# Optimization experiments

Hardware: AMD Instinct MI355X
Metric: run time of the kernel (lower is better)

Reference implementation:

```python
import jax, jax.numpy as jnp
import numpy as np

B, S, NX, H = 8, 1024, 1024, 16
D = NX // H  # head_features = 64
SCALE = True


def setup_inputs() -> dict:
    key = jax.random.key(0)
    k1, k2, k3 = jax.random.split(key, 3)
    x = jax.random.normal(k1, (B, S, NX), dtype=jnp.float32)
    w_attn = jax.random.normal(k2, (NX, 3 * NX), dtype=jnp.float32) * 0.02
    b_attn = jnp.zeros((3 * NX,), dtype=jnp.float32)
    w_proj = jax.random.normal(k3, (NX, NX), dtype=jnp.float32) * 0.02
    b_proj = jnp.zeros((NX,), dtype=jnp.float32)
    return {"x": x, "w_attn": w_attn, "b_attn": b_attn, "w_proj": w_proj, "b_proj": b_proj}


def _split_heads(t):
    # (B, S, NX) -> (B, H, S, D)
    return t.reshape(B, S, H, D).transpose(0, 2, 1, 3)


def reference(x, w_attn, b_attn, w_proj, b_proj):
    # fused QKV projection (Conv1D): addmm over flattened tokens
    qkv = x @ w_attn + b_attn                      # (B, S, 3*NX)
    q, k, v = jnp.split(qkv, 3, axis=-1)
    q = _split_heads(q)                            # (B, H, S, D)
    k = _split_heads(k)
    v = _split_heads(v)

    w = jnp.einsum("bhqd,bhkd->bhqk", q, k)        # full S x S scores
    if SCALE:
        w = w / jnp.sqrt(jnp.asarray(D, w.dtype))
    # causal mask applied exactly as in the source: multiply + big-negative subtract
    b = jnp.tril(jnp.ones((S, S), dtype=w.dtype))[None, None]
    w = w * b - 1e10 * (1.0 - b)
    w = jax.nn.softmax(w, axis=-1)                 # attn_pdrop = 0 (eval)
    a = jnp.einsum("bhqk,bhkd->bhqd", w, v)        # (B, H, S, D)

    # merge heads: (B, H, S, D) -> (B, S, NX)
    a = a.transpose(0, 2, 1, 3).reshape(B, S, NX)
    a = a @ w_proj + b_proj                        # c_proj; resid_pdrop = 0 (eval)
    return a
```

## Files before the change

kernel.cpp:

```cpp
#include <hip/hip_runtime.h>
#include <hip/hip_bf16.h>

#define BB 8
#define SS 1024
#define NXX 1024
#define HH 16
#define DD 64
#define MM (BB * SS)

typedef __attribute__((ext_vector_type(8))) short short8;
typedef __attribute__((ext_vector_type(4))) short short4v;
typedef __attribute__((ext_vector_type(4))) float float4v;

static __device__ inline short bf16bits(float v) {
    __hip_bfloat16 t = __float2bfloat16(v);
    return *reinterpret_cast<short*>(&t);
}

__global__ __launch_bounds__(256) void prep_kernel(
    const float* __restrict__ x, __hip_bfloat16* __restrict__ xb,
    const float* __restrict__ w_attn, __hip_bfloat16* __restrict__ wT_attn,
    const float* __restrict__ w_proj, __hip_bfloat16* __restrict__ wT_proj)
{
    __shared__ __hip_bfloat16 tile[32][33];
    const int blk = blockIdx.x;
    const int tid = threadIdx.x;

    if (blk < 8192) {
        int i = blk * 1024 + tid * 4;
        float4 v = *(const float4*)(x + i);
        xb[i + 0] = __float2bfloat16(v.x);
        xb[i + 1] = __float2bfloat16(v.y);
        xb[i + 2] = __float2bfloat16(v.z);
        xb[i + 3] = __float2bfloat16(v.w);
        return;
    }
    const float* W;
    __hip_bfloat16* Wt;
    int K, N, idx;
    if (blk < 8192 + 3072) { idx = blk - 8192;  W = w_attn; Wt = wT_attn; K = NXX; N = 3 * NXX; }
    else                   { idx = blk - 11264; W = w_proj; Wt = wT_proj; K = NXX; N = NXX; }
    const int k0 = (idx % (K / 32)) * 32;
    const int n0 = (idx / (K / 32)) * 32;
    const int tx = tid % 32;
    const int ty = tid / 32;
#pragma unroll
    for (int p = 0; p < 4; ++p) {
        int k = ty + p * 8;
        tile[k][tx] = __float2bfloat16(W[(size_t)(k0 + k) * N + n0 + tx]);
    }
    __syncthreads();
#pragma unroll
    for (int p = 0; p < 4; ++p) {
        int nn = ty + p * 8;
        Wt[(size_t)(n0 + nn) * K + k0 + tx] = tile[tx][nn];
    }
}

#define STAGE_A(DST, kk)                                                       \
    {                                                                          \
        _Pragma("unroll") for (int j_ = 0; j_ < LA; ++j_) {                    \
            const __hip_bfloat16* s_ = aSrc + (size_t)(j_ * 128) * K + (kk);   \
            char* d_ = (char*)(DST) + j_ * 8192 + (wave << 10);                \
            __builtin_amdgcn_global_load_lds(                                  \
                (const __attribute__((address_space(1))) void*)s_,             \
                (__attribute__((address_space(3))) void*)d_, 16, 0, 0);        \
        }                                                                      \
    }

#define STAGE_B(DST, kk)                                                       \
    {                                                                          \
        _Pragma("unroll") for (int j_ = 0; j_ < LB; ++j_) {                    \
            const __hip_bfloat16* s_ = bSrc + (size_t)(j_ * 128) * K + (kk);   \
            char* d_ = (char*)(DST) + j_ * 8192 + (wave << 10);                \
            __builtin_amdgcn_global_load_lds(                                  \
                (const __attribute__((address_space(1))) void*)s_,             \
                (__attribute__((address_space(3))) void*)d_, 16, 0, 0);        \
        }                                                                      \
    }

#define WAIT_LGKM0_FENCED()                                                    \
    asm volatile("s_waitcnt lgkmcnt(0)" ::: "memory");                         \
    __builtin_amdgcn_sched_barrier(0);

#define WAIT_VMCNT_LT()                                                        \
    if constexpr (LT == 3) { asm volatile("s_waitcnt vmcnt(3)" ::: "memory"); }\
    else                   { asm volatile("s_waitcnt vmcnt(2)" ::: "memory"); }

template <int MODE, int BM, int BN>
__global__ __launch_bounds__(512, 2) void gemm256(
    const __hip_bfloat16* __restrict__ A,
    const __hip_bfloat16* __restrict__ Bt,
    const float* __restrict__ bias,
    void* __restrict__ Cv,
    __hip_bfloat16* __restrict__ vT,
    int M, int K, int N)
{
    constexpr int NWM = BM / 64;
    constexpr int NWN = 8 / NWM;
    constexpr int WCOLS = BN / NWN;
    constexpr int NF = WCOLS / 16;
    constexpr int ASZ = BM * 64;
    constexpr int BSZ = BN * 64;
    constexpr int LA = BM / 128;
    constexpr int LB = BN / 128;
    constexpr int LT = LA + LB;

    __shared__ __attribute__((aligned(16))) char smem[3 * ASZ + 2 * BSZ];

    const int tid  = threadIdx.x;
    const int wave = tid >> 6;
    const int lane = tid & 63;
    const int wm = (wave / NWN) * 64;
    const int wn = (wave % NWN) * WCOLS;

    const int nwg = (int)gridDim.x;
    const int cpx = nwg >> 3;
    const int bid = (int)blockIdx.x;
    const int swz = (bid & 7) * cpx + (bid >> 3);
    const int ntN = N / BN;
    const int width = ntN << 3;
    const int group = swz / width;
    const int w = swz % width;
    const int m0 = (group * 8 + (w & 7)) * BM;
    const int n0 = (w >> 3) * BN;

    const int NT = K >> 5;

    const int row_s  = tid >> 2;
    const int srccol = (((tid & 3) ^ ((tid >> 3) & 3)) << 3);
    const __hip_bfloat16* aSrc = A  + (size_t)(m0 + row_s) * K + srccol;
    const __hip_bfloat16* bSrc = Bt + (size_t)(n0 + row_s) * K + srccol;

    const int l15 = lane & 15, q4 = lane >> 4;
    const int sslot = (q4 ^ ((l15 >> 1) & 3)) << 4;
    const int offA = (wm + l15) * 64 + sslot;
    const int offB = (wn + l15) * 64 + sslot;

    float4v acc[4][NF];
#pragma unroll
    for (int i = 0; i < 4; ++i)
#pragma unroll
        for (int j = 0; j < NF; ++j) acc[i][j] = (float4v){0.f, 0.f, 0.f, 0.f};

    char* const Abuf0 = (char*)smem;
    char* const Bbuf0 = (char*)smem + 3 * ASZ;

    STAGE_A(Abuf0,       0);
    STAGE_B(Bbuf0,       0);
    STAGE_A(Abuf0 + ASZ, 32);
    STAGE_B(Bbuf0 + BSZ, 32);
    WAIT_VMCNT_LT();
    __builtin_amdgcn_s_barrier();

    int ia = 0;
    for (int t = 0; t < NT; ++t) {
        const char* Ab = Abuf0 + ia * ASZ;
        char* Bb = Bbuf0 + (t & 1) * BSZ;
        const int ia2 = (ia == 0) ? 2 : ia - 1;

        short8 a[4], b[NF];

#pragma unroll
        for (int mf = 0; mf < 2; ++mf) a[mf] = *(const short8*)(Ab + offA + mf * 1024);
#pragma unroll
        for (int nf = 0; nf < NF; ++nf) b[nf] = *(const short8*)(Bb + offB + nf * 1024);
        if (t + 2 < NT) STAGE_A(Abuf0 + ia2 * ASZ, (t + 2) << 5);
        __builtin_amdgcn_s_barrier();
        WAIT_LGKM0_FENCED();
        __builtin_amdgcn_s_setprio(1);
#pragma unroll
        for (int mf = 0; mf < 2; ++mf)
#pragma unroll
            for (int nf = 0; nf < NF; ++nf)
                acc[mf][nf] = __builtin_amdgcn_mfma_f32_16x16x32_bf16(
                    a[mf], b[nf], acc[mf][nf], 0, 0, 0);
        __builtin_amdgcn_s_setprio(0);
        __builtin_amdgcn_s_barrier();

#pragma unroll
        for (int mf = 2; mf < 4; ++mf) a[mf] = *(const short8*)(Ab + offA + mf * 1024);
        if (t + 2 < NT) {
            STAGE_B(Bb, (t + 2) << 5);
            WAIT_VMCNT_LT();
        } else if (t + 1 < NT) {
            asm volatile("s_waitcnt vmcnt(0)" ::: "memory");
        }
        __builtin_amdgcn_s_barrier();
        WAIT_LGKM0_FENCED();
        __builtin_amdgcn_s_setprio(1);
#pragma unroll
        for (int mf = 2; mf < 4; ++mf)
#pragma unroll
            for (int nf = 0; nf < NF; ++nf)
                acc[mf][nf] = __builtin_amdgcn_mfma_f32_16x16x32_bf16(
                    a[mf], b[nf], acc[mf][nf], 0, 0, 0);
        __builtin_amdgcn_s_setprio(0);
        __builtin_amdgcn_s_barrier();

        ia = (ia == 2) ? 0 : ia + 1;
    }

    const int cr = q4 * 4;
    const int cc = l15;

    if (MODE == 1 && n0 >= 2048) {
        const int bb = m0 / SS;
#pragma unroll
        for (int mf = 0; mf < 4; ++mf) {
            int grow = m0 + wm + mf * 16 + cr;
            int ssr = grow & (SS - 1);
#pragma unroll
            for (int nf = 0; nf < NF; ++nf) {
                int gcol = n0 + wn + nf * 16 + cc;
                float bv = bias[gcol];
                int col = gcol - 2048;
                int hh = col >> 6, dd = col & 63;
                short4v pk;
#pragma unroll
                for (int r = 0; r < 4; ++r) pk[r] = bf16bits(acc[mf][nf][r] + bv);
                *(short4v*)(vT + (size_t)((bb * HH + hh) * 64 + dd) * SS + ssr) = pk;
            }
        }
    } else {
        const float qs = (MODE == 1 && n0 < 1024) ? 0.125f : 1.0f;
#pragma unroll
        for (int mf = 0; mf < 4; ++mf) {
            int grow = m0 + wm + mf * 16 + cr;
#pragma unroll
            for (int nf = 0; nf < NF; ++nf) {
                int gcol = n0 + wn + nf * 16 + cc;
                float bv = bias[gcol];
#pragma unroll
                for (int r = 0; r < 4; ++r) {
                    float v = (acc[mf][nf][r] + bv) * qs;
                    if constexpr (MODE == 1)
                        ((__hip_bfloat16*)Cv)[(size_t)(grow + r) * N + gcol] =
                            __float2bfloat16(v);
                    else
                        ((float*)Cv)[(size_t)(grow + r) * N + gcol] = v;
                }
            }
        }
    }
}

#define PSTR 72

__global__ __launch_bounds__(256) void attn_mfma_kernel(
    const __hip_bfloat16* __restrict__ qkv,
    const __hip_bfloat16* __restrict__ vT,
    __hip_bfloat16* __restrict__ aout)
{
    const int bh = blockIdx.x;
    const int b = bh / HH, h = bh % HH;
    const int q0 = ((int)gridDim.y - 1 - (int)blockIdx.y) * 128;

    __shared__ __hip_bfloat16 Ks[64 * PSTR];
    __shared__ __hip_bfloat16 Vs[64 * PSTR];
    __shared__ __hip_bfloat16 Ps[4][32 * PSTR];

    const int tid  = threadIdx.x;
    const int wave = tid >> 6;
    const int lane = tid & 63;
    const int quad = lane >> 4;
    const int l16  = lane & 15;

    short8 qf[2][2];
#pragma unroll
    for (int t = 0; t < 2; ++t) {
        const __hip_bfloat16* qp = qkv +
            (size_t)(b * SS + q0 + wave * 32 + t * 16 + l16) * 3072 + h * 64 + quad * 8;
        qf[t][0] = *(const short8*)qp;
        qf[t][1] = *(const short8*)(qp + 32);
    }

    float4v o_acc[2][4];
    float l_acc[2][4];
#pragma unroll
    for (int t = 0; t < 2; ++t)
#pragma unroll
        for (int nt = 0; nt < 4; ++nt) o_acc[t][nt] = (float4v){0.f, 0.f, 0.f, 0.f};
#pragma unroll
    for (int t = 0; t < 2; ++t)
#pragma unroll
        for (int r = 0; r < 4; ++r) l_acc[t][r] = 0.f;

    const int sk  = tid & 63;
    const int sdo = (tid >> 6) * 16;
    const int vd  = tid >> 2;
    const int vko = (tid & 3) * 16;
    const int qmin_w = q0 + wave * 32;
    const int nkt = q0 / 64 + 2;

    for (int kt = 0; kt < nkt; ++kt) {
        const int k0 = kt * 64;
        __syncthreads();
        {
            const __hip_bfloat16* kr =
                qkv + (size_t)(b * SS + k0 + sk) * 3072 + 1024 + h * 64 + sdo;
            *(short8*)&Ks[sk * PSTR + sdo]     = *(const short8*)kr;
            *(short8*)&Ks[sk * PSTR + sdo + 8] = *(const short8*)(kr + 8);
            const __hip_bfloat16* vr = vT + (size_t)(bh * 64 + vd) * SS + k0 + vko;
            *(short8*)&Vs[vd * PSTR + vko]     = *(const short8*)vr;
            *(short8*)&Vs[vd * PSTR + vko + 8] = *(const short8*)(vr + 8);
        }
        __syncthreads();
        if (k0 > qmin_w + 31) continue;

        const short* ks = (const short*)Ks;
        float4v sacc[2][4];
#pragma unroll
        for (int t = 0; t < 2; ++t)
#pragma unroll
            for (int nt = 0; nt < 4; ++nt) sacc[t][nt] = (float4v){0.f, 0.f, 0.f, 0.f};
#pragma unroll
        for (int kc = 0; kc < 2; ++kc)
#pragma unroll
            for (int nt = 0; nt < 4; ++nt) {
                short8 kb = *(const short8*)(ks + (nt * 16 + l16) * PSTR + kc * 32 + quad * 8);
                sacc[0][nt] = __builtin_amdgcn_mfma_f32_16x16x32_bf16(qf[0][kc], kb, sacc[0][nt], 0, 0, 0);
                sacc[1][nt] = __builtin_amdgcn_mfma_f32_16x16x32_bf16(qf[1][kc], kb, sacc[1][nt], 0, 0, 0);
            }

        const bool needmask = (k0 + 63 > qmin_w);
        __hip_bfloat16* pw = Ps[wave];
#pragma unroll
        for (int t = 0; t < 2; ++t)
#pragma unroll
            for (int nt = 0; nt < 4; ++nt) {
                int kk = k0 + nt * 16 + l16;
#pragma unroll
                for (int r = 0; r < 4; ++r) {
                    float s = sacc[t][nt][r];
                    if (needmask) {
                        int qq = qmin_w + t * 16 + quad * 4 + r;
                        if (kk > qq) s = -1e10f;
                    }
                    float p = __expf(s);
                    l_acc[t][r] += p;
                    pw[(t * 16 + quad * 4 + r) * PSTR + nt * 16 + l16] =
                        __float2bfloat16(p);
                }
            }

        const short* ps = (const short*)pw;
        const short* vs = (const short*)Vs;
#pragma unroll
        for (int kc = 0; kc < 2; ++kc) {
            short8 pa0 = *(const short8*)(ps + (0 * 16 + l16) * PSTR + kc * 32 + quad * 8);
            short8 pa1 = *(const short8*)(ps + (1 * 16 + l16) * PSTR + kc * 32 + quad * 8);
#pragma unroll
            for (int nt = 0; nt < 4; ++nt) {
                short8 vb = *(const short8*)(vs + (nt * 16 + l16) * PSTR + kc * 32 + quad * 8);
                o_acc[0][nt] = __builtin_amdgcn_mfma_f32_16x16x32_bf16(pa0, vb, o_acc[0][nt], 0, 0, 0);
                o_acc[1][nt] = __builtin_amdgcn_mfma_f32_16x16x32_bf16(pa1, vb, o_acc[1][nt], 0, 0, 0);
            }
        }
    }

#pragma unroll
    for (int t = 0; t < 2; ++t)
#pragma unroll
        for (int r = 0; r < 4; ++r) {
            float l = l_acc[t][r];
            l += __shfl_xor(l, 1);
            l += __shfl_xor(l, 2);
            l += __shfl_xor(l, 4);
            l += __shfl_xor(l, 8);
            float inv = 1.f / l;
            int row = q0 + wave * 32 + t * 16 + quad * 4 + r;
            __hip_bfloat16* op = aout + (size_t)(b * SS + row) * NXX + h * 64 + l16;
#pragma unroll
            for (int nt = 0; nt < 4; ++nt)
                op[nt * 16] = __float2bfloat16(o_acc[t][nt][r] * inv);
        }
}

extern "C" void kernel_launch(void* const* d_in, const int* in_sizes, int n_in,
                              void* d_out, int out_size, void* d_ws, size_t ws_size,
                              hipStream_t stream)
{
    const float* x      = (const float*)d_in[0];
    const float* w_attn = (const float*)d_in[1];
    const float* b_attn = (const float*)d_in[2];
    const float* w_proj = (const float*)d_in[3];
    const float* b_proj = (const float*)d_in[4];
    float* out = (float*)d_out;

    char* ws = (char*)d_ws;
    __hip_bfloat16* qkv     = (__hip_bfloat16*)ws;
    __hip_bfloat16* vT      = (__hip_bfloat16*)(ws + (size_t)48 * 1024 * 1024);
    __hip_bfloat16* xb      = (__hip_bfloat16*)(ws + (size_t)64 * 1024 * 1024);
    __hip_bfloat16* amid    = xb;
    __hip_bfloat16* wT_attn = (__hip_bfloat16*)(ws + (size_t)80 * 1024 * 1024);
    __hip_bfloat16* wT_proj = (__hip_bfloat16*)(ws + (size_t)86 * 1024 * 1024);

    prep_kernel<<<dim3(12288), dim3(256), 0, stream>>>(
        x, xb, w_attn, wT_attn, w_proj, wT_proj);

    gemm256<1, 256, 128><<<dim3((MM / 256) * ((3 * NXX) / 128)), dim3(512), 0, stream>>>(
        xb, wT_attn, b_attn, qkv, vT, MM, NXX, 3 * NXX);

    attn_mfma_kernel<<<dim3(BB * HH, SS / 128), dim3(256), 0, stream>>>(qkv, vT, amid);

    gemm256<0, 128, 128><<<dim3((MM / 128) * (NXX / 128)), dim3(512), 0, stream>>>(
        amid, wT_proj, b_proj, out, nullptr, MM, NXX, NXX);
}
```

Baseline: 221.7 us.

## Add 256x256 ping-pong GEMM for QKV projection and enlarge proj tile

Adds a new gemm8k kernel that computes 256x256 output tiles with 128KB of dynamic LDS, double-buffered global_load_lds staging, interleaved quarter-step MFMA phases with barriers and setprio, and an XCD-aware block swizzle. It replaces the 256x128 QKV projection GEMM when the dynamic shared-memory attribute can be set. The output projection switches from 128x128 to 256x128 tiles. The aim is more operand reuse per LDS load and better overlap of loads with MFMA; the cost is fewer workgroups, possibly lower occupancy, and more barriers per iteration.

```diff
diff --git a/kernel.cpp b/kernel.cpp
--- a/kernel.cpp
+++ b/kernel.cpp
@@ -57,6 +57,10 @@
     }
 }
 
+#define WAIT_LGKM0_FENCED()                                                    \
+    asm volatile("s_waitcnt lgkmcnt(0)" ::: "memory");                         \
+    __builtin_amdgcn_sched_barrier(0);
+
 #define STAGE_A(DST, kk)                                                       \
     {                                                                          \
         _Pragma("unroll") for (int j_ = 0; j_ < LA; ++j_) {                    \
@@ -78,10 +82,6 @@
                 (__attribute__((address_space(3))) void*)d_, 16, 0, 0);        \
         }                                                                      \
     }
-
-#define WAIT_LGKM0_FENCED()                                                    \
-    asm volatile("s_waitcnt lgkmcnt(0)" ::: "memory");                         \
-    __builtin_amdgcn_sched_barrier(0);
 
 #define WAIT_VMCNT_LT()                                                        \
     if constexpr (LT == 3) { asm volatile("s_waitcnt vmcnt(3)" ::: "memory"); }\
@@ -245,6 +245,203 @@
     }
 }
 
+#define STAGE8(SRCBASE, DST, half, kk)                                         \
+    {                                                                          \
+        _Pragma("unroll") for (int j_ = 0; j_ < 2; ++j_) {                     \
+            const __hip_bfloat16* s_ =                                         \
+                (SRCBASE) + (size_t)((half) * 128 + j_ * 64) * K + (kk);       \
+            char* d_ = (char*)(DST) + (half) * 16384 + j_ * 8192 + (wave << 10); \
+            __builtin_amdgcn_global_load_lds(                                  \
+                (const __attribute__((address_space(1))) void*)s_,             \
+                (__attribute__((address_space(3))) void*)d_, 16, 0, 0);        \
+        }                                                                      \
+    }
+
+template <int MODE>
+__global__ __launch_bounds__(512, 2) void gemm8k(
+    const __hip_bfloat16* __restrict__ A,
+    const __hip_bfloat16* __restrict__ Bt,
+    const float* __restrict__ bias,
+    void* __restrict__ Cv,
+    __hip_bfloat16* __restrict__ vT,
+    int M, int K, int N)
+{
+    extern __shared__ char smem[];
+
+    const int tid  = threadIdx.x;
+    const int wave = tid >> 6;
+    const int lane = tid & 63;
+    const int wr = wave >> 2;
+    const int wc = wave & 3;
+
+    const int nwg = (int)gridDim.x;
+    const int cpx = nwg >> 3;
+    const int bid = (int)blockIdx.x;
+    const int swz = (bid & 7) * cpx + (bid >> 3);
+    const int ntN = N >> 8;
+    const int width = ntN << 3;
+    const int group = swz / width;
+    const int w = swz % width;
+    const int m0 = ((group << 3) + (w & 7)) << 8;
+    const int n0 = (w >> 3) << 8;
+
+    const int NT = K >> 6;
+
+    const int row_s  = tid >> 3;
+    const int slot_s = tid & 7;
+    const int srccol = ((slot_s ^ (row_s & 7)) << 3);
+    const __hip_bfloat16* aSrc = A  + (size_t)(m0 + row_s) * K + srccol;
+    const __hip_bfloat16* bSrc = Bt + (size_t)(n0 + row_s) * K + srccol;
+
+    const int l15 = lane & 15, q4 = lane >> 4, xr = lane & 7;
+    const int sl0 = (q4 ^ xr) << 4;
+    const int sl1 = ((4 + q4) ^ xr) << 4;
+    const int offA0 = ((wr << 7) + l15) * 128 + sl0;
+    const int offA1 = ((wr << 7) + l15) * 128 + sl1;
+    const int offB0 = ((wc << 6) + l15) * 128 + sl0;
+    const int offB1 = ((wc << 6) + l15) * 128 + sl1;
+
+    float4v acc[8][4];
+#pragma unroll
+    for (int i = 0; i < 8; ++i)
+#pragma unroll
+        for (int j = 0; j < 4; ++j) acc[i][j] = (float4v){0.f, 0.f, 0.f, 0.f};
+
+    STAGE8(aSrc, smem, 0, 0);
+    STAGE8(aSrc, smem, 1, 0);
+    STAGE8(bSrc, smem + 32768, 0, 0);
+    STAGE8(bSrc, smem + 32768, 1, 0);
+    if (NT > 1) {
+        STAGE8(bSrc, smem + 65536 + 32768, 0, 64);
+        STAGE8(bSrc, smem + 65536 + 32768, 1, 64);
+        asm volatile("s_waitcnt vmcnt(4)" ::: "memory");
+    } else {
+        asm volatile("s_waitcnt vmcnt(0)" ::: "memory");
+    }
+    __builtin_amdgcn_s_barrier();
+
+    for (int t = 0; t < NT; ++t) {
+        const char* Ab = smem + ((t & 1) << 16);
+        const char* Bb = Ab + 32768;
+        char* AbN = (char*)smem + (((t + 1) & 1) << 16);
+        char* BbC = (char*)Ab + 32768;
+
+        short8 a0[4], a1[4], b0[4], b1[4];
+
+#pragma unroll
+        for (int mf = 0; mf < 4; ++mf) a0[mf] = *(const short8*)(Ab + offA0 + mf * 2048);
+#pragma unroll
+        for (int nf = 0; nf < 4; ++nf) b0[nf] = *(const short8*)(Bb + offB0 + nf * 2048);
+        if (t + 1 < NT) STAGE8(aSrc, AbN, 0, (t + 1) << 6);
+        __builtin_amdgcn_s_barrier();
+        WAIT_LGKM0_FENCED();
+        __builtin_amdgcn_s_setprio(1);
+#pragma unroll
+        for (int mf = 0; mf < 4; ++mf)
+#pragma unroll
+            for (int nf = 0; nf < 4; ++nf)
+                acc[mf][nf] = __builtin_amdgcn_mfma_f32_16x16x32_bf16(
+                    a0[mf], b0[nf], acc[mf][nf], 0, 0, 0);
+        __builtin_amdgcn_s_setprio(0);
+        __builtin_amdgcn_s_barrier();
+
+#pragma unroll
+        for (int mf = 0; mf < 4; ++mf) a1[mf] = *(const short8*)(Ab + offA1 + mf * 2048);
+#pragma unroll
+        for (int nf = 0; nf < 4; ++nf) b1[nf] = *(const short8*)(Bb + offB1 + nf * 2048);
+        if (t + 1 < NT) STAGE8(aSrc, AbN, 1, (t + 1) << 6);
+        __builtin_amdgcn_s_barrier();
+        WAIT_LGKM0_FENCED();
+        __builtin_amdgcn_s_setprio(1);
+#pragma unroll
+        for (int mf = 0; mf < 4; ++mf)
+#pragma unroll
+            for (int nf = 0; nf < 4; ++nf)
+                acc[mf][nf] = __builtin_amdgcn_mfma_f32_16x16x32_bf16(
+                    a1[mf], b1[nf], acc[mf][nf], 0, 0, 0);
+        __builtin_amdgcn_s_setprio(0);
+        __builtin_amdgcn_s_barrier();
+
+#pragma unroll
+        for (int mf = 0; mf < 4; ++mf) a0[mf] = *(const short8*)(Ab + offA0 + (mf + 4) * 2048);
+        if (t + 2 < NT) STAGE8(bSrc, BbC, 0, (t + 2) << 6);
+        __builtin_amdgcn_s_barrier();
+        WAIT_LGKM0_FENCED();
+        __builtin_amdgcn_s_setprio(1);
+#pragma unroll
+        for (int mf = 0; mf < 4; ++mf)
+#pragma unroll
+            for (int nf = 0; nf < 4; ++nf)
+                acc[mf + 4][nf] = __builtin_amdgcn_mfma_f32_16x16x32_bf16(
+                    a0[mf], b0[nf], acc[mf + 4][nf], 0, 0, 0);
+        __builtin_amdgcn_s_setprio(0);
+        __builtin_amdgcn_s_barrier();
+
+#pragma unroll
+        for (int mf = 0; mf < 4; ++mf) a1[mf] = *(const short8*)(Ab + offA1 + (mf + 4) * 2048);
+        if (t + 2 < NT) {
+            STAGE8(bSrc, BbC, 1, (t + 2) << 6);
+            asm volatile("s_waitcnt vmcnt(4)" ::: "memory");
+        } else if (t + 1 < NT) {
+            asm volatile("s_waitcnt vmcnt(0)" ::: "memory");
+        }
+        __builtin_amdgcn_s_barrier();
+        WAIT_LGKM0_FENCED();
+        __builtin_amdgcn_s_setprio(1);
+#pragma unroll
+        for (int mf = 0; mf < 4; ++mf)
+#pragma unroll
+            for (int nf = 0; nf < 4; ++nf)
+                acc[mf + 4][nf] = __builtin_amdgcn_mfma_f32_16x16x32_bf16(
+                    a1[mf], b1[nf], acc[mf + 4][nf], 0, 0, 0);
+        __builtin_amdgcn_s_setprio(0);
+        __builtin_amdgcn_s_barrier();
+    }
+
+    const int cr = q4 * 4;
+    const int cc = l15;
+
+    if (MODE == 1 && n0 >= 2048) {
+        const int bb = m0 / SS;
+#pragma unroll
+        for (int mf = 0; mf < 8; ++mf) {
+            int grow = m0 + (wr << 7) + mf * 16 + cr;
+            int ssr = grow & (SS - 1);
+#pragma unroll
+            for (int nf = 0; nf < 4; ++nf) {
+                int gcol = n0 + (wc << 6) + nf * 16 + cc;
+                float bv = bias[gcol];
+                int col = gcol - 2048;
+                int hh = col >> 6, dd = col & 63;
+                short4v pk;
+#pragma unroll
+                for (int r = 0; r < 4; ++r) pk[r] = bf16bits(acc[mf][nf][r] + bv);
+                *(short4v*)(vT + (size_t)((bb * HH + hh) * 64 + dd) * SS + ssr) = pk;
+            }
+        }
+    } else {
+        const float qs = (MODE == 1 && n0 < 1024) ? 0.125f : 1.0f;
+#pragma unroll
+        for (int mf = 0; mf < 8; ++mf) {
+            int grow = m0 + (wr << 7) + mf * 16 + cr;
+#pragma unroll
+            for (int nf = 0; nf < 4; ++nf) {
+                int gcol = n0 + (wc << 6) + nf * 16 + cc;
+                float bv = bias[gcol];
+#pragma unroll
+                for (int r = 0; r < 4; ++r) {
+                    float v = (acc[mf][nf][r] + bv) * qs;
+                    if constexpr (MODE == 1)
+                        ((__hip_bfloat16*)Cv)[(size_t)(grow + r) * N + gcol] =
+                            __float2bfloat16(v);
+                    else
+                        ((float*)Cv)[(size_t)(grow + r) * N + gcol] = v;
+                }
+            }
+        }
+    }
+}
+
 #define PSTR 72
 
 __global__ __launch_bounds__(256) void attn_mfma_kernel(
@@ -396,14 +593,28 @@
     __hip_bfloat16* wT_attn = (__hip_bfloat16*)(ws + (size_t)80 * 1024 * 1024);
     __hip_bfloat16* wT_proj = (__hip_bfloat16*)(ws + (size_t)86 * 1024 * 1024);
 
+    static int dyn_state = 0;
+    if (dyn_state == 0) {
+        hipError_t e = hipFuncSetAttribute(
+            reinterpret_cast<const void*>(&gemm8k<1>),
+            hipFuncAttributeMaxDynamicSharedMemorySize, 131072);
+        dyn_state = (e == hipSuccess) ? 1 : -1;
+        (void)hipGetLastError();
+    }
+
     prep_kernel<<<dim3(12288), dim3(256), 0, stream>>>(
         x, xb, w_attn, wT_attn, w_proj, wT_proj);
 
-    gemm256<1, 256, 128><<<dim3((MM / 256) * ((3 * NXX) / 128)), dim3(512), 0, stream>>>(
-        xb, wT_attn, b_attn, qkv, vT, MM, NXX, 3 * NXX);
+    if (dyn_state == 1) {
+        gemm8k<1><<<dim3((MM / 256) * ((3 * NXX) / 256)), dim3(512), 131072, stream>>>(
+            xb, wT_attn, b_attn, qkv, vT, MM, NXX, 3 * NXX);
+    } else {
+        gemm256<1, 256, 128><<<dim3((MM / 256) * ((3 * NXX) / 128)), dim3(512), 0, stream>>>(
+            xb, wT_attn, b_attn, qkv, vT, MM, NXX, 3 * NXX);
+    }
 
     attn_mfma_kernel<<<dim3(BB * HH, SS / 128), dim3(256), 0, stream>>>(qkv, vT, amid);
 
-    gemm256<0, 128, 128><<<dim3((MM / 128) * (NXX / 128)), dim3(512), 0, stream>>>(
+    gemm256<0, 256, 128><<<dim3((MM / 256) * (NXX / 128)), dim3(512), 0, stream>>>(
         amid, wT_proj, b_proj, out, nullptr, MM, NXX, NXX);
 }
```

Measured after the change: 229.6 us. 1.04x slower.

## Add triple-buffered dynamic-LDS GEMM with single barrier pair per K-step

Applied to the files above, without the earlier changes.

Introduces a new GEMM kernel that uses three LDS stages, allocated as dynamic shared memory, prefetching two K-tiles ahead through global_load_lds. Each K-tile is loaded into registers before the next prefetch is issued, which aims to hide global memory latency better than the previous pipeline. The output projection also switches from 128x128 to 256x128 tiles, halving its grid. The larger LDS footprint may limit blocks per CU, and the runtime falls back to the old kernel if the attribute call fails.

```diff
diff --git a/kernel.cpp b/kernel.cpp
--- a/kernel.cpp
+++ b/kernel.cpp
@@ -57,6 +57,10 @@
     }
 }
 
+#define WAIT_LGKM0_FENCED()                                                    \
+    asm volatile("s_waitcnt lgkmcnt(0)" ::: "memory");                         \
+    __builtin_amdgcn_sched_barrier(0);
+
 #define STAGE_A(DST, kk)                                                       \
     {                                                                          \
         _Pragma("unroll") for (int j_ = 0; j_ < LA; ++j_) {                    \
@@ -79,9 +83,148 @@
         }                                                                      \
     }
 
-#define WAIT_LGKM0_FENCED()                                                    \
-    asm volatile("s_waitcnt lgkmcnt(0)" ::: "memory");                         \
-    __builtin_amdgcn_sched_barrier(0);
+template <int MODE, int BM, int BN>
+__global__ __launch_bounds__(512, 2) void gemm3b(
+    const __hip_bfloat16* __restrict__ A,
+    const __hip_bfloat16* __restrict__ Bt,
+    const float* __restrict__ bias,
+    void* __restrict__ Cv,
+    __hip_bfloat16* __restrict__ vT,
+    int M, int K, int N)
+{
+    constexpr int NWM = BM / 64;
+    constexpr int NWN = 8 / NWM;
+    constexpr int WCOLS = BN / NWN;
+    constexpr int NF = WCOLS / 16;
+    constexpr int ASZ = BM * 64;
+    constexpr int BSZ = BN * 64;
+    constexpr int LA = BM / 128;
+    constexpr int LB = BN / 128;
+
+    extern __shared__ __attribute__((aligned(16))) char smem[];
+
+    const int tid  = threadIdx.x;
+    const int wave = tid >> 6;
+    const int lane = tid & 63;
+    const int wm = (wave / NWN) * 64;
+    const int wn = (wave % NWN) * WCOLS;
+
+    const int nwg = (int)gridDim.x;
+    const int cpx = nwg >> 3;
+    const int bid = (int)blockIdx.x;
+    const int swz = (bid & 7) * cpx + (bid >> 3);
+    const int ntN = N / BN;
+    const int width = ntN << 3;
+    const int group = swz / width;
+    const int w = swz % width;
+    const int m0 = (group * 8 + (w & 7)) * BM;
+    const int n0 = (w >> 3) * BN;
+
+    const int NT = K >> 5;
+
+    const int row_s  = tid >> 2;
+    const int srccol = (((tid & 3) ^ ((tid >> 3) & 3)) << 3);
+    const __hip_bfloat16* aSrc = A  + (size_t)(m0 + row_s) * K + srccol;
+    const __hip_bfloat16* bSrc = Bt + (size_t)(n0 + row_s) * K + srccol;
+
+    const int l15 = lane & 15, q4 = lane >> 4;
+    const int sslot = (q4 ^ ((l15 >> 1) & 3)) << 4;
+    const int offA = (wm + l15) * 64 + sslot;
+    const int offB = (wn + l15) * 64 + sslot;
+
+    float4v acc[4][NF];
+#pragma unroll
+    for (int i = 0; i < 4; ++i)
+#pragma unroll
+        for (int j = 0; j < NF; ++j) acc[i][j] = (float4v){0.f, 0.f, 0.f, 0.f};
+
+    char* const Abuf0 = (char*)smem;
+    char* const Bbuf0 = (char*)smem + 3 * ASZ;
+
+    STAGE_A(Abuf0,       0);
+    STAGE_B(Bbuf0,       0);
+    STAGE_A(Abuf0 + ASZ, 32);
+    STAGE_B(Bbuf0 + BSZ, 32);
+    asm volatile("s_waitcnt vmcnt(3)" ::: "memory");
+    __builtin_amdgcn_s_barrier();
+
+    int ia = 0;
+    for (int t = 0; t < NT; ++t) {
+        const char* Ab = Abuf0 + ia * ASZ;
+        const char* Bb = Bbuf0 + ia * BSZ;
+        const int ia2 = (ia >= 1) ? ia - 1 : 2;
+
+        short8 a[4], b[NF];
+#pragma unroll
+        for (int mf = 0; mf < 4; ++mf) a[mf] = *(const short8*)(Ab + offA + mf * 1024);
+#pragma unroll
+        for (int nf = 0; nf < NF; ++nf) b[nf] = *(const short8*)(Bb + offB + nf * 1024);
+
+        if (t + 2 < NT) {
+            STAGE_A(Abuf0 + ia2 * ASZ, (t + 2) << 5);
+            STAGE_B(Bbuf0 + ia2 * BSZ, (t + 2) << 5);
+            asm volatile("s_waitcnt vmcnt(3)" ::: "memory");
+        } else if (t + 1 < NT) {
+            asm volatile("s_waitcnt vmcnt(0)" ::: "memory");
+        }
+        __builtin_amdgcn_s_barrier();
+        WAIT_LGKM0_FENCED();
+        __builtin_amdgcn_s_setprio(1);
+#pragma unroll
+        for (int mf = 0; mf < 4; ++mf)
+#pragma unroll
+            for (int nf = 0; nf < NF; ++nf)
+                acc[mf][nf] = __builtin_amdgcn_mfma_f32_16x16x32_bf16(
+                    a[mf], b[nf], acc[mf][nf], 0, 0, 0);
+        __builtin_amdgcn_s_setprio(0);
+        __builtin_amdgcn_s_barrier();
+
+        ia = (ia == 2) ? 0 : ia + 1;
+    }
+
+    const int cr = q4 * 4;
+    const int cc = l15;
+
+    if (MODE == 1 && n0 >= 2048) {
+        const int bb = m0 / SS;
+#pragma unroll
+        for (int mf = 0; mf < 4; ++mf) {
+            int grow = m0 + wm + mf * 16 + cr;
+            int ssr = grow & (SS - 1);
+#pragma unroll
+            for (int nf = 0; nf < NF; ++nf) {
+                int gcol = n0 + wn + nf * 16 + cc;
+                float bv = bias[gcol];
+                int col = gcol - 2048;
+                int hh = col >> 6, dd = col & 63;
+                short4v pk;
+#pragma unroll
+                for (int r = 0; r < 4; ++r) pk[r] = bf16bits(acc[mf][nf][r] + bv);
+                *(short4v*)(vT + (size_t)((bb * HH + hh) * 64 + dd) * SS + ssr) = pk;
+            }
+        }
+    } else {
+        const float qs = (MODE == 1 && n0 < 1024) ? 0.125f : 1.0f;
+#pragma unroll
+        for (int mf = 0; mf < 4; ++mf) {
+            int grow = m0 + wm + mf * 16 + cr;
+#pragma unroll
+            for (int nf = 0; nf < NF; ++nf) {
+                int gcol = n0 + wn + nf * 16 + cc;
+                float bv = bias[gcol];
+#pragma unroll
+                for (int r = 0; r < 4; ++r) {
+                    float v = (acc[mf][nf][r] + bv) * qs;
+                    if constexpr (MODE == 1)
+                        ((__hip_bfloat16*)Cv)[(size_t)(grow + r) * N + gcol] =
+                            __float2bfloat16(v);
+                    else
+                        ((float*)Cv)[(size_t)(grow + r) * N + gcol] = v;
+                }
+            }
+        }
+    }
+}
 
 #define WAIT_VMCNT_LT()                                                        \
     if constexpr (LT == 3) { asm volatile("s_waitcnt vmcnt(3)" ::: "memory"); }\
@@ -396,14 +539,39 @@
     __hip_bfloat16* wT_attn = (__hip_bfloat16*)(ws + (size_t)80 * 1024 * 1024);
     __hip_bfloat16* wT_proj = (__hip_bfloat16*)(ws + (size_t)86 * 1024 * 1024);
 
+    constexpr int DYN_LDS = 3 * (256 * 64) + 3 * (128 * 64);
+    static int dyn_state = 0;
+    if (dyn_state == 0) {
+        hipError_t e1 = hipFuncSetAttribute(
+            reinterpret_cast<const void*>(&gemm3b<1, 256, 128>),
+            hipFuncAttributeMaxDynamicSharedMemorySize, DYN_LDS);
+        hipError_t e2 = hipFuncSetAttribute(
+            reinterpret_cast<const void*>(&gemm3b<0, 256, 128>),
+            hipFuncAttributeMaxDynamicSharedMemorySize, DYN_LDS);
+        dyn_state = (e1 == hipSuccess && e2 == hipSuccess) ? 1 : -1;
+        (void)hipGetLastError();
+    }
+
     prep_kernel<<<dim3(12288), dim3(256), 0, stream>>>(
         x, xb, w_attn, wT_attn, w_proj, wT_proj);
 
-    gemm256<1, 256, 128><<<dim3((MM / 256) * ((3 * NXX) / 128)), dim3(512), 0, stream>>>(
-        xb, wT_attn, b_attn, qkv, vT, MM, NXX, 3 * NXX);
+    if (dyn_state == 1) {
+        gemm3b<1, 256, 128><<<dim3((MM / 256) * ((3 * NXX) / 128)), dim3(512),
+                              DYN_LDS, stream>>>(
+            xb, wT_attn, b_attn, qkv, vT, MM, NXX, 3 * NXX);
+    } else {
+        gemm256<1, 256, 128><<<dim3((MM / 256) * ((3 * NXX) / 128)), dim3(512), 0, stream>>>(
+            xb, wT_attn, b_attn, qkv, vT, MM, NXX, 3 * NXX);
+    }
 
     attn_mfma_kernel<<<dim3(BB * HH, SS / 128), dim3(256), 0, stream>>>(qkv, vT, amid);
 
-    gemm256<0, 128, 128><<<dim3((MM / 128) * (NXX / 128)), dim3(512), 0, stream>>>(
-        amid, wT_proj, b_proj, out, nullptr, MM, NXX, NXX);
+    if (dyn_state == 1) {
+        gemm3b<0, 256, 128><<<dim3((MM / 256) * (NXX / 128)), dim3(512),
+                              DYN_LDS, stream>>>(
+            amid, wT_proj, b_proj, out, nullptr, MM, NXX, NXX);
+    } else {
+        gemm256<0, 256, 128><<<dim3((MM / 256) * (NXX / 128)), dim3(512), 0, stream>>>(
+            amid, wT_proj, b_proj, out, nullptr, MM, NXX, NXX);
+    }
 }
```

Result: faster. 216.2 us (-2.5%).
